# Kernel tuning notes

Hardware: AMD Instinct MI355X
Metric: run time of the kernel (lower is better)

## Reference

```python
import jax, jax.numpy as jnp
import numpy as np

N_NODES = 1_000_000
N_EDGES = 32_000_000
DC = 16
HIDDEN = 32
EPS = 1e-8
LN_EPS = 1e-5


def _harmonic_encoding(x, dC):
    # x: [n] curvature in [-1,1]; returns [n, dC] (dC even here)
    norm = jnp.clip((x + 1.0) / (2.0 + EPS), 0.0, 1.0)
    freqs = jnp.arange(1, dC // 2 + 1, dtype=x.dtype) * jnp.pi  # [dC/2]
    ang = norm[:, None] * freqs[None, :]                        # [n, dC/2]
    # interleave sin/cos exactly like torch.stack(...,dim=2).view(n,dC)
    return jnp.stack([jnp.sin(ang), jnp.cos(ang)], axis=2).reshape(x.shape[0], dC)


def setup_inputs() -> dict:
    key = jax.random.key(0)
    k_orc, k_ei, k_w1, k_w2, k_g = jax.random.split(key, 5)
    node_orc = jax.random.uniform(k_orc, (N_NODES,), dtype=jnp.float32) * 2.0 - 1.0
    edge_index = jax.random.randint(k_ei, (2, N_EDGES), 0, N_NODES, dtype=jnp.int64)
    # MLP params (torch Linear convention: W [out, in])
    W1 = jax.random.normal(k_w1, (HIDDEN, DC), dtype=jnp.float32) * (1.0 / np.sqrt(DC))
    b1 = jnp.zeros((HIDDEN,), dtype=jnp.float32)
    W2 = jax.random.normal(k_w2, (DC, HIDDEN), dtype=jnp.float32) * (1.0 / np.sqrt(HIDDEN))
    b2 = jnp.zeros((DC,), dtype=jnp.float32)
    gamma = jnp.ones((DC,), dtype=jnp.float32)
    beta = jnp.zeros((DC,), dtype=jnp.float32)
    return {"node_orc": node_orc, "edge_index": edge_index,
            "W1": W1, "b1": b1, "W2": W2, "b2": b2,
            "gamma": gamma, "beta": beta}


def _neighbor_mean(node_orc, edge_index):
    src, dst = edge_index[0], edge_index[1]
    n = node_orc.shape[0]
    deg = jnp.zeros((n,), node_orc.dtype).at[src].add(1.0).at[dst].add(1.0)
    s = (jnp.zeros((n,), node_orc.dtype)
         .at[src].add(node_orc[dst])
         .at[dst].add(node_orc[src]))
    return jnp.where(deg > 0, s / jnp.where(deg > 0, deg, 1.0), 0.0)


def reference(node_orc, edge_index, W1, b1, W2, b2, gamma, beta):
    # advanced harmonic encoding: node encoding + neighbor-mean encoding
    nb_mean = _neighbor_mean(node_orc, edge_index)
    Phi_base = jnp.concatenate(
        [_harmonic_encoding(node_orc, DC // 2),
         _harmonic_encoding(nb_mean, DC // 2)], axis=1)      # [n, 16]
    # learnable MLP (dropout in eval = identity) + LayerNorm + residual
    h = jax.nn.relu(jnp.einsum('nd,hd->nh', Phi_base, W1) + b1)
    y = jnp.einsum('nh,dh->nd', h, W2) + b2
    mu = jnp.mean(y, axis=-1, keepdims=True)
    var = jnp.var(y, axis=-1, keepdims=True)
    y = (y - mu) / jnp.sqrt(var + LN_EPS) * gamma + beta
    return y + Phi_base
```

## Files before the change

kernel.cpp:

```cpp
#include <hip/hip_runtime.h>
#include <hip/hip_bf16.h>

constexpr int kNodes = 1000000;
constexpr int kEdges = 32000000;

constexpr int NB = 256;
constexpr int BSHIFT = 12;
constexpr int BNODES = 4096;
constexpr int NBUSED = (kNodes + BNODES - 1) / BNODES;
constexpr int EPT = 4096;
constexpr int TILES = (kEdges + EPT - 1) / EPT;
constexpr int TSTRIDE = 8960;

constexpr size_t kRecBytes = (size_t)TILES * TSTRIDE * 4;
constexpr size_t kTblOff   = kRecBytes;
constexpr size_t kTblBytes = ((size_t)(NB + 1) * TILES * 2 + 15) & ~(size_t)15;
constexpr size_t kAccOff   = kTblOff + kTblBytes;
constexpr size_t kWsNeeded = kAccOff + (size_t)kNodes * 8;

__global__ __launch_bounds__(512) void scatter_sort(
        const int* __restrict__ ei, const float* __restrict__ orc,
        unsigned* __restrict__ rec, unsigned short* __restrict__ tbl) {
    __shared__ alignas(16) int es[EPT];
    __shared__ alignas(16) int ed[EPT];
    __shared__ alignas(16) unsigned reorder[TSTRIDE];
    __shared__ unsigned cnt[NB];
    __shared__ unsigned scanbuf[NB];
    const int tid = threadIdx.x;
    const int t = blockIdx.x;
    const int e0 = t * EPT;
    const int ne = min(EPT, kEdges - e0);

    for (int k = tid; k < NB; k += 512) cnt[k] = 0u;
    for (int k = tid; k < TSTRIDE; k += 512) reorder[k] = 0xFFFFFFFFu;
    __syncthreads();

    for (int k4 = tid * 4; k4 < ne; k4 += 2048) {
        const int4 s4 = *reinterpret_cast<const int4*>(ei + e0 + k4);
        const int4 d4 = *reinterpret_cast<const int4*>(ei + kEdges + e0 + k4);
        *reinterpret_cast<int4*>(es + k4) = s4;
        *reinterpret_cast<int4*>(ed + k4) = d4;
        atomicAdd(&cnt[s4.x >> BSHIFT], 1u);
        atomicAdd(&cnt[s4.y >> BSHIFT], 1u);
        atomicAdd(&cnt[s4.z >> BSHIFT], 1u);
        atomicAdd(&cnt[s4.w >> BSHIFT], 1u);
        atomicAdd(&cnt[d4.x >> BSHIFT], 1u);
        atomicAdd(&cnt[d4.y >> BSHIFT], 1u);
        atomicAdd(&cnt[d4.z >> BSHIFT], 1u);
        atomicAdd(&cnt[d4.w >> BSHIFT], 1u);
    }
    __syncthreads();

    if (tid < NB) scanbuf[tid] = (cnt[tid] + 3u) & ~3u;
    __syncthreads();
    for (int off = 1; off < NB; off <<= 1) {
        unsigned v = 0u;
        if (tid < NB && tid >= off) v = scanbuf[tid - off];
        __syncthreads();
        if (tid < NB) scanbuf[tid] += v;
        __syncthreads();
    }
    if (tid < NB) {
        const unsigned pc = (cnt[tid] + 3u) & ~3u;
        const unsigned st = scanbuf[tid] - pc;
        tbl[(size_t)tid * TILES + t] = (unsigned short)st;
        cnt[tid] = st;
    }
    if (tid == 0) tbl[(size_t)NB * TILES + t] = (unsigned short)scanbuf[NB - 1];
    __syncthreads();

    for (int k4 = tid * 4; k4 < ne; k4 += 2048) {
        #pragma unroll
        for (int j = 0; j < 4; ++j) {
            const int k = k4 + j;
            const int s = es[k], d = ed[k];
            const float os = orc[s], od = orc[d];
            unsigned qs = __float2uint_rn((od + 1.0f) * 524288.0f);
            unsigned qd = __float2uint_rn((os + 1.0f) * 524288.0f);
            qs = qs > 0xFFFFFu ? 0xFFFFFu : qs;
            qd = qd > 0xFFFFFu ? 0xFFFFFu : qd;
            const unsigned rs = atomicAdd(&cnt[s >> BSHIFT], 1u);
            reorder[rs] = ((unsigned)(s & (BNODES - 1)) << 20) | qs;
            const unsigned rd = atomicAdd(&cnt[d >> BSHIFT], 1u);
            reorder[rd] = ((unsigned)(d & (BNODES - 1)) << 20) | qd;
        }
    }
    __syncthreads();

    const unsigned total = scanbuf[NB - 1];
    unsigned* __restrict__ g = rec + (size_t)t * TSTRIDE;
    for (unsigned k = tid * 4; k < total; k += 2048)
        *reinterpret_cast<int4*>(g + k) = *reinterpret_cast<const int4*>(reorder + k);
}

__global__ __launch_bounds__(512) void bucket_accum(
        const unsigned* __restrict__ rec, const unsigned short* __restrict__ tbl,
        unsigned long long* __restrict__ acc) {
    __shared__ unsigned long long lacc[BNODES];
    const int b = blockIdx.x;
    const int tid = threadIdx.x;
    for (int k = tid; k < BNODES; k += 512) lacc[k] = 0ull;
    __syncthreads();
    const unsigned short* __restrict__ r0 = tbl + (size_t)b * TILES;
    const unsigned short* __restrict__ r1 = tbl + (size_t)(b + 1) * TILES;
    for (int t = tid; t < TILES; t += 512) {
        const unsigned st = r0[t];
        const unsigned en = r1[t];
        const uint4* __restrict__ p =
            reinterpret_cast<const uint4*>(rec + (size_t)t * TSTRIDE + st);
        const unsigned n4 = (en - st) >> 2;
        for (unsigned i = 0; i < n4; ++i) {
            const uint4 v = p[i];
            const unsigned long long a0 = (v.x == 0xFFFFFFFFu) ? 0ull
                : ((1ull << 42) | (unsigned long long)(v.x & 0xFFFFFu));
            atomicAdd(&lacc[v.x >> 20], a0);
            const unsigned long long a1 = (v.y == 0xFFFFFFFFu) ? 0ull
                : ((1ull << 42) | (unsigned long long)(v.y & 0xFFFFFu));
            atomicAdd(&lacc[v.y >> 20], a1);
            const unsigned long long a2 = (v.z == 0xFFFFFFFFu) ? 0ull
                : ((1ull << 42) | (unsigned long long)(v.z & 0xFFFFFu));
            atomicAdd(&lacc[v.z >> 20], a2);
            const unsigned long long a3 = (v.w == 0xFFFFFFFFu) ? 0ull
                : ((1ull << 42) | (unsigned long long)(v.w & 0xFFFFFu));
            atomicAdd(&lacc[v.w >> 20], a3);
        }
    }
    __syncthreads();
    const int base = b << BSHIFT;
    for (int k = tid; k < BNODES; k += 512) {
        const int n = base + k;
        if (n < kNodes) acc[n] = lacc[k];
    }
}

constexpr float kScale = 1048576.0f;
constexpr float kInvScale = 1.0f / 1048576.0f;
constexpr long long kBias = 1ll << 36;

__global__ __launch_bounds__(256) void zero_acc(unsigned long long* __restrict__ acc) {
    int i = blockIdx.x * 256 + threadIdx.x;
    if (i < kNodes) acc[i] = 0ull;
}

__global__ __launch_bounds__(256) void edge_kernel(
        const int* __restrict__ ei,
        const float* __restrict__ orc,
        unsigned long long* __restrict__ acc) {
    int t = blockIdx.x * 256 + threadIdx.x;
    int e0 = t * 4;
    if (e0 >= kEdges) return;
    const int4 s4 = *reinterpret_cast<const int4*>(ei + e0);
    const int4 d4 = *reinterpret_cast<const int4*>(ei + kEdges + e0);
    const int ss[4] = {s4.x, s4.y, s4.z, s4.w};
    const int dd[4] = {d4.x, d4.y, d4.z, d4.w};
    #pragma unroll
    for (int k = 0; k < 4; ++k) {
        const float os = orc[ss[k]];
        const float od = orc[dd[k]];
        const unsigned long long ps =
            (1ull << 48) + (unsigned long long)(kBias + (long long)__float2ll_rn(od * kScale));
        const unsigned long long pd =
            (1ull << 48) + (unsigned long long)(kBias + (long long)__float2ll_rn(os * kScale));
        atomicAdd(&acc[ss[k]], ps);
        atomicAdd(&acc[dd[k]], pd);
    }
}

template <int MODE>
__global__ __launch_bounds__(256) void node_kernel(
        const float* __restrict__ orc,
        const unsigned long long* __restrict__ acc,
        const float* __restrict__ W1, const float* __restrict__ b1,
        const float* __restrict__ W2, const float* __restrict__ b2,
        const float* __restrict__ gamma, const float* __restrict__ beta,
        float* __restrict__ out) {
    const int i = blockIdx.x * 256 + threadIdx.x;
    if (i >= kNodes) return;

    const float x0 = orc[i];
    const unsigned long long p = acc[i];
    float nb;
    if (MODE == 0) {
        const unsigned deg = (unsigned)(p >> 48);
        const long long sf = (long long)(p & ((1ull << 48) - 1)) - (long long)deg * kBias;
        const float s = (float)sf * kInvScale;
        nb = (deg > 0) ? s / (float)deg : 0.0f;
    } else {
        const unsigned deg = (unsigned)(p >> 42);
        const unsigned long long sumq = p & ((1ull << 42) - 1);
        nb = (deg > 0) ? ((float)sumq * (1.0f / 524288.0f) / (float)deg - 1.0f) : 0.0f;
    }

    constexpr float kPi = 3.14159265358979323846f;
    float Phi[16];
    const float n0 = __saturatef((x0 + 1.0f) * 0.5f);
    const float n1 = __saturatef((nb + 1.0f) * 0.5f);
    #pragma unroll
    for (int k = 0; k < 4; ++k) {
        const float a0 = n0 * (float)(k + 1) * kPi;
        const float a1 = n1 * (float)(k + 1) * kPi;
        Phi[2 * k]     = __sinf(a0);
        Phi[2 * k + 1] = __cosf(a0);
        Phi[8 + 2 * k]     = __sinf(a1);
        Phi[8 + 2 * k + 1] = __cosf(a1);
    }

    float y[16];
    #pragma unroll
    for (int d = 0; d < 16; ++d) y[d] = b2[d];
    #pragma unroll
    for (int j = 0; j < 32; ++j) {
        float a = b1[j];
        #pragma unroll
        for (int d = 0; d < 16; ++d) a = fmaf(Phi[d], W1[j * 16 + d], a);
        a = fmaxf(a, 0.0f);
        #pragma unroll
        for (int d = 0; d < 16; ++d) y[d] = fmaf(a, W2[d * 32 + j], y[d]);
    }

    float mu = 0.0f;
    #pragma unroll
    for (int d = 0; d < 16; ++d) mu += y[d];
    mu *= (1.0f / 16.0f);
    float var = 0.0f;
    #pragma unroll
    for (int d = 0; d < 16; ++d) { const float t = y[d] - mu; var = fmaf(t, t, var); }
    var *= (1.0f / 16.0f);
    const float inv = rsqrtf(var + 1e-5f);

    float4* o4 = reinterpret_cast<float4*>(out + (size_t)i * 16);
    #pragma unroll
    for (int q = 0; q < 4; ++q) {
        float4 o;
        o.x = (y[4 * q + 0] - mu) * inv * gamma[4 * q + 0] + beta[4 * q + 0] + Phi[4 * q + 0];
        o.y = (y[4 * q + 1] - mu) * inv * gamma[4 * q + 1] + beta[4 * q + 1] + Phi[4 * q + 1];
        o.z = (y[4 * q + 2] - mu) * inv * gamma[4 * q + 2] + beta[4 * q + 2] + Phi[4 * q + 2];
        o.w = (y[4 * q + 3] - mu) * inv * gamma[4 * q + 3] + beta[4 * q + 3] + Phi[4 * q + 3];
        o4[q] = o;
    }
}

extern "C" void kernel_launch(void* const* d_in, const int* in_sizes, int n_in,
                              void* d_out, int out_size, void* d_ws, size_t ws_size,
                              hipStream_t stream) {
    const float* orc   = (const float*)d_in[0];
    const int*   ei    = (const int*)d_in[1];
    const float* W1    = (const float*)d_in[2];
    const float* b1    = (const float*)d_in[3];
    const float* W2    = (const float*)d_in[4];
    const float* b2    = (const float*)d_in[5];
    const float* gamma = (const float*)d_in[6];
    const float* beta  = (const float*)d_in[7];
    float* out = (float*)d_out;
    char* ws = (char*)d_ws;

    if (ws_size >= kWsNeeded) {
        unsigned* rec = (unsigned*)ws;
        unsigned short* tbl = (unsigned short*)(ws + kTblOff);
        unsigned long long* acc = (unsigned long long*)(ws + kAccOff);
        scatter_sort<<<TILES, 512, 0, stream>>>(ei, orc, rec, tbl);
        bucket_accum<<<NBUSED, 512, 0, stream>>>(rec, tbl, acc);
        node_kernel<2><<<(kNodes + 255) / 256, 256, 0, stream>>>(
            orc, acc, W1, b1, W2, b2, gamma, beta, out);
    } else {
        unsigned long long* acc = (unsigned long long*)ws;
        zero_acc<<<(kNodes + 255) / 256, 256, 0, stream>>>(acc);
        edge_kernel<<<(kEdges / 4 + 255) / 256, 256, 0, stream>>>(ei, orc, acc);
        node_kernel<0><<<(kNodes + 255) / 256, 256, 0, stream>>>(
            orc, acc, W1, b1, W2, b2, gamma, beta, out);
    }
}
```

Baseline: 863.3 us.

## Split bucket accumulation across tile ranges and drop edge staging in LDS

The bucket accumulation grid gains a second dimension so each bucket's tiles are split across four blocks. Each block writes its own partial accumulator array, and the node kernel sums the four partials. This targets the low parallelism of about 245 blocks on a large GPU. The scatter-sort kernel no longer stages edge indices in shared memory; it re-reads them from global memory, which frees LDS for higher occupancy (launch bounds now request 8 blocks). The node kernel derives the harmonic features from one hardware sin/cos via angle-addition identities, which adds some floating-point error.

```diff
diff --git a/kernel.cpp b/kernel.cpp
--- a/kernel.cpp
+++ b/kernel.cpp
@@ -11,18 +11,18 @@
 constexpr int EPT = 4096;
 constexpr int TILES = (kEdges + EPT - 1) / EPT;
 constexpr int TSTRIDE = 8960;
+constexpr int SSPLIT = 4;
+constexpr int TPS = (TILES + SSPLIT - 1) / SSPLIT;
 
 constexpr size_t kRecBytes = (size_t)TILES * TSTRIDE * 4;
 constexpr size_t kTblOff   = kRecBytes;
 constexpr size_t kTblBytes = ((size_t)(NB + 1) * TILES * 2 + 15) & ~(size_t)15;
 constexpr size_t kAccOff   = kTblOff + kTblBytes;
-constexpr size_t kWsNeeded = kAccOff + (size_t)kNodes * 8;
-
-__global__ __launch_bounds__(512) void scatter_sort(
+constexpr size_t kWsNeeded = kAccOff + (size_t)SSPLIT * kNodes * 8;
+
+__global__ __launch_bounds__(512, 8) void scatter_sort(
         const int* __restrict__ ei, const float* __restrict__ orc,
         unsigned* __restrict__ rec, unsigned short* __restrict__ tbl) {
-    __shared__ alignas(16) int es[EPT];
-    __shared__ alignas(16) int ed[EPT];
     __shared__ alignas(16) unsigned reorder[TSTRIDE];
     __shared__ unsigned cnt[NB];
     __shared__ unsigned scanbuf[NB];
@@ -38,8 +38,6 @@
     for (int k4 = tid * 4; k4 < ne; k4 += 2048) {
         const int4 s4 = *reinterpret_cast<const int4*>(ei + e0 + k4);
         const int4 d4 = *reinterpret_cast<const int4*>(ei + kEdges + e0 + k4);
-        *reinterpret_cast<int4*>(es + k4) = s4;
-        *reinterpret_cast<int4*>(ed + k4) = d4;
         atomicAdd(&cnt[s4.x >> BSHIFT], 1u);
         atomicAdd(&cnt[s4.y >> BSHIFT], 1u);
         atomicAdd(&cnt[s4.z >> BSHIFT], 1u);
@@ -70,15 +68,20 @@
     __syncthreads();
 
     for (int k4 = tid * 4; k4 < ne; k4 += 2048) {
+        const int4 s4 = *reinterpret_cast<const int4*>(ei + e0 + k4);
+        const int4 d4 = *reinterpret_cast<const int4*>(ei + kEdges + e0 + k4);
+        const int ss[4] = {s4.x, s4.y, s4.z, s4.w};
+        const int dd[4] = {d4.x, d4.y, d4.z, d4.w};
+        float osv[4], odv[4];
+        #pragma unroll
+        for (int j = 0; j < 4; ++j) { osv[j] = orc[ss[j]]; odv[j] = orc[dd[j]]; }
         #pragma unroll
         for (int j = 0; j < 4; ++j) {
-            const int k = k4 + j;
-            const int s = es[k], d = ed[k];
-            const float os = orc[s], od = orc[d];
-            unsigned qs = __float2uint_rn((od + 1.0f) * 524288.0f);
-            unsigned qd = __float2uint_rn((os + 1.0f) * 524288.0f);
+            unsigned qs = __float2uint_rn((odv[j] + 1.0f) * 524288.0f);
+            unsigned qd = __float2uint_rn((osv[j] + 1.0f) * 524288.0f);
             qs = qs > 0xFFFFFu ? 0xFFFFFu : qs;
             qd = qd > 0xFFFFFu ? 0xFFFFFu : qd;
+            const int s = ss[j], d = dd[j];
             const unsigned rs = atomicAdd(&cnt[s >> BSHIFT], 1u);
             reorder[rs] = ((unsigned)(s & (BNODES - 1)) << 20) | qs;
             const unsigned rd = atomicAdd(&cnt[d >> BSHIFT], 1u);
@@ -93,17 +96,20 @@
         *reinterpret_cast<int4*>(g + k) = *reinterpret_cast<const int4*>(reorder + k);
 }
 
-__global__ __launch_bounds__(512) void bucket_accum(
+__global__ __launch_bounds__(512, 8) void bucket_accum(
         const unsigned* __restrict__ rec, const unsigned short* __restrict__ tbl,
         unsigned long long* __restrict__ acc) {
     __shared__ unsigned long long lacc[BNODES];
     const int b = blockIdx.x;
+    const int s = blockIdx.y;
     const int tid = threadIdx.x;
     for (int k = tid; k < BNODES; k += 512) lacc[k] = 0ull;
     __syncthreads();
+    const int t0 = s * TPS;
+    const int t1 = min(t0 + TPS, TILES);
     const unsigned short* __restrict__ r0 = tbl + (size_t)b * TILES;
     const unsigned short* __restrict__ r1 = tbl + (size_t)(b + 1) * TILES;
-    for (int t = tid; t < TILES; t += 512) {
+    for (int t = t0 + tid; t < t1; t += 512) {
         const unsigned st = r0[t];
         const unsigned en = r1[t];
         const uint4* __restrict__ p =
@@ -126,10 +132,11 @@
         }
     }
     __syncthreads();
+    unsigned long long* __restrict__ ap = acc + (size_t)s * kNodes;
     const int base = b << BSHIFT;
     for (int k = tid; k < BNODES; k += 512) {
         const int n = base + k;
-        if (n < kNodes) acc[n] = lacc[k];
+        if (n < kNodes) ap[n] = lacc[k];
     }
 }
 
@@ -178,31 +185,41 @@
     if (i >= kNodes) return;
 
     const float x0 = orc[i];
-    const unsigned long long p = acc[i];
-    float nb;
+    float n1;
     if (MODE == 0) {
+        const unsigned long long p = acc[i];
         const unsigned deg = (unsigned)(p >> 48);
         const long long sf = (long long)(p & ((1ull << 48) - 1)) - (long long)deg * kBias;
-        const float s = (float)sf * kInvScale;
-        nb = (deg > 0) ? s / (float)deg : 0.0f;
+        const float nb = (deg > 0) ? ((float)sf * kInvScale) / (float)deg : 0.0f;
+        n1 = __saturatef((nb + 1.0f) * 0.5f);
     } else {
+        unsigned long long p = acc[i];
+        #pragma unroll
+        for (int s = 1; s < SSPLIT; ++s) p += acc[(size_t)s * kNodes + i];
         const unsigned deg = (unsigned)(p >> 42);
         const unsigned long long sumq = p & ((1ull << 42) - 1);
-        nb = (deg > 0) ? ((float)sumq * (1.0f / 524288.0f) / (float)deg - 1.0f) : 0.0f;
-    }
-
-    constexpr float kPi = 3.14159265358979323846f;
+        n1 = (deg > 0) ? __fdividef((float)sumq, (float)deg * 1048576.0f) : 0.5f;
+    }
+    const float n0 = __saturatef((x0 + 1.0f) * 0.5f);
+
     float Phi[16];
-    const float n0 = __saturatef((x0 + 1.0f) * 0.5f);
-    const float n1 = __saturatef((nb + 1.0f) * 0.5f);
-    #pragma unroll
-    for (int k = 0; k < 4; ++k) {
-        const float a0 = n0 * (float)(k + 1) * kPi;
-        const float a1 = n1 * (float)(k + 1) * kPi;
-        Phi[2 * k]     = __sinf(a0);
-        Phi[2 * k + 1] = __cosf(a0);
-        Phi[8 + 2 * k]     = __sinf(a1);
-        Phi[8 + 2 * k + 1] = __cosf(a1);
+    {
+        const float s1 = __builtin_amdgcn_sinf(n0 * 0.5f);
+        const float c1 = __builtin_amdgcn_cosf(n0 * 0.5f);
+        const float s2 = 2.0f * s1 * c1, c2 = fmaf(-2.0f * s1, s1, 1.0f);
+        const float s3 = s1 * c2 + c1 * s2, c3 = c1 * c2 - s1 * s2;
+        const float s4 = 2.0f * s2 * c2, c4 = fmaf(-2.0f * s2, s2, 1.0f);
+        Phi[0] = s1; Phi[1] = c1; Phi[2] = s2; Phi[3] = c2;
+        Phi[4] = s3; Phi[5] = c3; Phi[6] = s4; Phi[7] = c4;
+    }
+    {
+        const float s1 = __builtin_amdgcn_sinf(n1 * 0.5f);
+        const float c1 = __builtin_amdgcn_cosf(n1 * 0.5f);
+        const float s2 = 2.0f * s1 * c1, c2 = fmaf(-2.0f * s1, s1, 1.0f);
+        const float s3 = s1 * c2 + c1 * s2, c3 = c1 * c2 - s1 * s2;
+        const float s4 = 2.0f * s2 * c2, c4 = fmaf(-2.0f * s2, s2, 1.0f);
+        Phi[8] = s1; Phi[9] = c1; Phi[10] = s2; Phi[11] = c2;
+        Phi[12] = s3; Phi[13] = c3; Phi[14] = s4; Phi[15] = c4;
     }
 
     float y[16];
@@ -259,7 +276,7 @@
         unsigned short* tbl = (unsigned short*)(ws + kTblOff);
         unsigned long long* acc = (unsigned long long*)(ws + kAccOff);
         scatter_sort<<<TILES, 512, 0, stream>>>(ei, orc, rec, tbl);
-        bucket_accum<<<NBUSED, 512, 0, stream>>>(rec, tbl, acc);
+        bucket_accum<<<dim3(NBUSED, SSPLIT), 512, 0, stream>>>(rec, tbl, acc);
         node_kernel<2><<<(kNodes + 255) / 256, 256, 0, stream>>>(
             orc, acc, W1, b1, W2, b2, gamma, beta, out);
     } else {
```

After: 895.5 us. 3.7% more time.
